# Performance work log

Hardware: AMD Instinct MI355X
Metric: run time of the kernel (lower is better)

Reference implementation:

```python
import jax, jax.numpy as jnp
import numpy as np
import math

H = 16          # num_heads
DN = 128        # qk_nope_head_dim
DR = 64         # qk_rope_head_dim
DV = 128        # v_head_dim
Q_LORA = 1536
KV_LORA = 512
EPS = 1e-6
ROPE_BASE = 10000.0
YARN_FACTOR = 16.0
ORIG_MAX = 8192


def rmsnorm(x, w):
    return x * jax.lax.rsqrt(jnp.mean(x * x, axis=-1, keepdims=True) + EPS) * w


def rotate_half(x):
    h = x.shape[-1] // 2
    return jnp.concatenate([-x[..., h:], x[..., :h]], axis=-1)


def yarn_cos_sin(L, dtype):
    # YaRN-scaled inverse frequencies (RotaryEmbedding defaults)
    pos2 = jnp.arange(0, DR, 2, dtype=jnp.float32)
    inv_freq = 1.0 / (ROPE_BASE ** (pos2 / DR))
    wavelen = 2.0 * jnp.pi / inv_freq
    # low_freq_factor=1.0, high_freq_factor=4.0
    ramp = jnp.clip((ORIG_MAX / wavelen - 1.0) / (4.0 - 1.0), 0.0, 1.0)
    inv_freq = inv_freq * (1.0 - ramp) + (inv_freq / YARN_FACTOR) * ramp
    t = jnp.arange(L, dtype=jnp.float32)
    freqs = jnp.outer(t, inv_freq)                      # [L, DR/2]
    emb = jnp.concatenate([freqs, freqs], axis=-1)      # [L, DR]
    attn_factor = 0.1 * math.log(YARN_FACTOR) + 1.0     # yarn attention scaling
    cos = (jnp.cos(emb) * attn_factor)[None, :, None, :].astype(dtype)
    sin = (jnp.sin(emb) * attn_factor)[None, :, None, :].astype(dtype)
    return cos, sin


def setup_inputs() -> dict:
    key = jax.random.key(0)
    ks = jax.random.split(key, 8)
    s = 0.02
    hid = 2048
    return {
        "x": jax.random.normal(ks[0], (2, 2048, hid), jnp.float32),
        "w_qa": jax.random.normal(ks[1], (hid, Q_LORA), jnp.float32) * s,
        "q_norm_w": jnp.ones((Q_LORA,), jnp.float32),
        "w_qb": jax.random.normal(ks[2], (Q_LORA, H * (DN + DR)), jnp.float32) * s,
        "w_kva": jax.random.normal(ks[3], (hid, KV_LORA + DR), jnp.float32) * s,
        "kv_norm_w": jnp.ones((KV_LORA,), jnp.float32),
        "w_kvb": jax.random.normal(ks[4], (KV_LORA, H * (DN + DV)), jnp.float32) * s,
        "w_o": jax.random.normal(ks[5], (H * DV, hid), jnp.float32) * s,
    }


def reference(x, w_qa, q_norm_w, w_qb, w_kva, kv_norm_w, w_kvb, w_o):
    B, L, _ = x.shape
    # --- low-rank Q path ---
    q = rmsnorm(x @ w_qa, q_norm_w) @ w_qb               # [B, L, H*(DN+DR)]
    q = q.reshape(B, L, H, DN + DR)
    q_nope, q_rope = q[..., :DN], q[..., DN:]
    # --- low-rank KV path ---
    kv = x @ w_kva                                       # [B, L, KV_LORA+DR]
    kv_c, k_rope = kv[..., :KV_LORA], kv[..., KV_LORA:]
    kv = rmsnorm(kv_c, kv_norm_w) @ w_kvb                # [B, L, H*(DN+DV)]
    kv = kv.reshape(B, L, H, DN + DV)
    k_nope, v = kv[..., :DN], kv[..., DN:]
    k_rope = jnp.broadcast_to(k_rope[:, :, None, :], (B, L, H, DR))
    # --- decoupled RoPE on rope sub-dims ---
    cos, sin = yarn_cos_sin(L, x.dtype)
    q_rope = q_rope * cos + rotate_half(q_rope) * sin
    k_rope = k_rope * cos + rotate_half(k_rope) * sin
    q = jnp.concatenate([q_nope, q_rope], axis=-1)       # [B, L, H, DN+DR]
    k = jnp.concatenate([k_nope, k_rope], axis=-1)
    # --- causal SDPA, scale = 1/sqrt(qk head dim) ---
    scale = 1.0 / math.sqrt(DN + DR)
    scores = jnp.einsum('blhd,bmhd->bhlm', q, k) * scale
    mask = jnp.tril(jnp.ones((L, L), bool))
    scores = jnp.where(mask[None, None], scores, jnp.array(-1e30, scores.dtype))
    attn = jax.nn.softmax(scores, axis=-1)
    out = jnp.einsum('bhlm,bmhd->blhd', attn, v)         # [B, L, H, DV]
    return out.reshape(B, L, H * DV) @ w_o               # [B, L, hidden]
```

## Files before the change

### kernel.cpp

```cpp
#include <hip/hip_runtime.h>
#include <hip/hip_bf16.h>
#include <math.h>

#define H_    16
#define B_    2
#define L_    2048
#define HID_  2048
#define QL_   1536
#define KVL_  512

typedef unsigned short u16;
typedef __attribute__((ext_vector_type(8))) short bf16x8;
typedef __attribute__((ext_vector_type(4))) float f32x4;

__device__ __forceinline__ float bf2f(u16 u) {
    unsigned int x = ((unsigned int)u) << 16;
    return __uint_as_float(x);
}
__device__ __forceinline__ u16 f2bf(float f) {
    __hip_bfloat16 b = __float2bfloat16(f);
    return *(u16*)&b;
}
__device__ __forceinline__ void g2l16(const void* g, void* l) {
    __builtin_amdgcn_global_load_lds(
        (const __attribute__((address_space(1))) unsigned int*)g,
        (__attribute__((address_space(3))) unsigned int*)l,
        16, 0, 0);
}
__device__ __forceinline__ int kswz(int l, int d) {
    return (((d >> 3) ^ (l & 7)) << 3) | (d & 7);
}

#define QSCALE (0.07216878364870323f * 1.4426950408889634f)

__device__ inline void yarn_cs(int l, int j, float& c, float& s)
{
    float invf = expf(-(float)(2 * j) * (9.210340371976184f / 64.f));
    float wavelen = 6.283185307179586f / invf;
    float ramp = (8192.f / wavelen - 1.f) * (1.f / 3.f);
    ramp = fminf(fmaxf(ramp, 0.f), 1.f);
    float invf2 = invf * (1.f - ramp) + invf * (1.f / 16.f) * ramp;
    float ang = (float)l * invf2;
    const float af = 1.2772588722239781f;
    c = cosf(ang) * af;
    s = sinf(ang) * af;
}

__global__ __launch_bounds__(256) void yarn_tab(float* __restrict__ tab)
{
    int idx = blockIdx.x * 256 + threadIdx.x;
    int l = idx >> 5, j = idx & 31;
    float c, s; yarn_cs(l, j, c, s);
    tab[l * 64 + j] = c;
    tab[l * 64 + 32 + j] = s;
}

__global__ __launch_bounds__(256) void cvt_bf16(
    const float* __restrict__ in, u16* __restrict__ outp)
{
    int idx = blockIdx.x * 256 + threadIdx.x;
    float4 a = ((const float4*)in)[idx * 2];
    float4 b = ((const float4*)in)[idx * 2 + 1];
    union { uint4 v; u16 s[8]; } u;
    u.s[0] = f2bf(a.x); u.s[1] = f2bf(a.y); u.s[2] = f2bf(a.z); u.s[3] = f2bf(a.w);
    u.s[4] = f2bf(b.x); u.s[5] = f2bf(b.y); u.s[6] = f2bf(b.z); u.s[7] = f2bf(b.w);
    ((uint4*)outp)[idx] = u.v;
}

__global__ __launch_bounds__(256) void wtrans(
    const float* __restrict__ W, u16* __restrict__ Wt, int K, int N,
    const float* __restrict__ wvec)
{
    __shared__ float t[64][65];
    const int n0 = blockIdx.x * 64, k0 = blockIdx.y * 64;
    const int tid = threadIdx.x;
    {
        int lr = tid >> 2, nc = (tid & 3) * 16;
        float wk = wvec ? wvec[k0 + lr] : 1.f;
        const float* src = W + (size_t)(k0 + lr) * N + n0 + nc;
#pragma unroll
        for (int j = 0; j < 16; j += 4) {
            float4 v = *(const float4*)(src + j);
            t[lr][nc + j] = v.x * wk; t[lr][nc + j + 1] = v.y * wk;
            t[lr][nc + j + 2] = v.z * wk; t[lr][nc + j + 3] = v.w * wk;
        }
    }
    __syncthreads();
    {
        int nr = tid >> 2, kc = (tid & 3) * 16;
        union { uint4 v[2]; u16 s[16]; } u;
#pragma unroll
        for (int j = 0; j < 16; ++j) u.s[j] = f2bf(t[kc + j][nr]);
        uint4* dst = (uint4*)(Wt + (size_t)(n0 + nr) * K + k0 + kc);
        dst[0] = u.v[0]; dst[1] = u.v[1];
    }
}

__global__ __launch_bounds__(256) void rowss(
    const u16* __restrict__ in, int stride, int ncols, float* __restrict__ sc)
{
    const int row = blockIdx.x, tid = threadIdx.x;
    const u16* ir = in + (size_t)row * stride;
    const int nch = ncols >> 3;
    float ss = 0.f;
    for (int c = tid; c < nch; c += 256) {
        union { uint4 v; u16 s[8]; } u;
        u.v = *(const uint4*)(ir + c * 8);
#pragma unroll
        for (int j = 0; j < 8; ++j) { float v = bf2f(u.s[j]); ss += v * v; }
    }
#pragma unroll
    for (int o = 32; o > 0; o >>= 1) ss += __shfl_xor(ss, o);
    __shared__ float red[4];
    if ((tid & 63) == 0) red[tid >> 6] = ss;
    __syncthreads();
    if (tid == 0) {
        float tot = red[0] + red[1] + red[2] + red[3];
        sc[row] = rsqrtf(tot / (float)ncols + 1e-6f);
    }
}

template<int NI> struct EpiStoreF32 {
    float* C; int ldc;
    __device__ void operator()(const f32x4* acc, int m0, int n0, int wr, int wc,
                               int g, int n) const {
#pragma unroll
        for (int mi = 0; mi < 4; ++mi)
#pragma unroll
            for (int ni = 0; ni < NI; ++ni)
#pragma unroll
                for (int i = 0; i < 4; ++i)
                    C[(size_t)(m0 + wr + mi * 16 + g * 4 + i) * ldc
                      + n0 + wc + ni * 16 + n] = acc[mi * NI + ni][i];
    }
};
struct EpiQA {
    u16* qaR; u16* kvf;
    __device__ void operator()(const f32x4* acc, int m0, int n0, int wr, int wc,
                               int g, int n) const {
        int c0 = n0 + wc;
#pragma unroll
        for (int mi = 0; mi < 4; ++mi)
#pragma unroll
            for (int i = 0; i < 4; ++i) {
                int rr = m0 + wr + mi * 16 + g * 4 + i;
#pragma unroll
                for (int ni = 0; ni < 4; ++ni) {
                    int c = c0 + ni * 16 + n;
                    float v = acc[mi * 4 + ni][i];
                    if (c < 1536)      qaR[(size_t)rr * 1536 + c] = f2bf(v);
                    else if (c < 2112) kvf[(size_t)rr * 576 + (c - 1536)] = f2bf(v);
                }
            }
    }
};
struct EpiQ {
    u16* Qb; const float* tab; const float* sc;
    __device__ void operator()(const f32x4* acc, int m0, int n0, int wr, int wc,
                               int g, int n) const {
        int c0 = n0 + wc;
        int h = c0 / 192, r0 = c0 % 192;
#pragma unroll
        for (int mi = 0; mi < 4; ++mi)
#pragma unroll
            for (int i = 0; i < 4; ++i) {
                int rr = m0 + wr + mi * 16 + g * 4 + i;
                int b = rr >> 11, l = rr & 2047;
                float scl = sc[rr] * QSCALE;
                size_t base = ((size_t)(b * 16 + h) * 2048 + l) * 192;
                if (r0 < 128) {
#pragma unroll
                    for (int ni = 0; ni < 4; ++ni)
                        Qb[base + r0 + ni * 16 + n] = f2bf(acc[mi * 4 + ni][i] * scl);
                } else {
#pragma unroll
                    for (int ni = 0; ni < 2; ++ni) {
                        int j = ni * 16 + n;
                        float cs = tab[l * 64 + j], sn = tab[l * 64 + 32 + j];
                        float lo = acc[mi * 4 + ni][i] * scl;
                        float hi = acc[mi * 4 + ni + 2][i] * scl;
                        Qb[base + 128 + j] = f2bf(lo * cs - hi * sn);
                        Qb[base + 160 + j] = f2bf(hi * cs + lo * sn);
                    }
                }
            }
    }
};
struct EpiKV {
    u16* Kb; u16* Vc; const float* sc;
    __device__ void operator()(const f32x4* acc, int m0, int n0, int wr, int wc,
                               int g, int n) const {
        int c0 = n0 + wc;
        int h = c0 >> 8, r0 = c0 & 255;
#pragma unroll
        for (int mi = 0; mi < 4; ++mi)
#pragma unroll
            for (int i = 0; i < 4; ++i) {
                int rr = m0 + wr + mi * 16 + g * 4 + i;
                int b = rr >> 11, l = rr & 2047;
                float scl = sc[rr];
                if (r0 < 128) {
                    size_t base = ((size_t)(b * 16 + h) * 2048 + l) * 192;
#pragma unroll
                    for (int ni = 0; ni < 4; ++ni) {
                        int d = r0 + ni * 16 + n;
                        Kb[base + kswz(l, d)] = f2bf(acc[mi * 4 + ni][i] * scl);
                    }
                } else {
#pragma unroll
                    for (int ni = 0; ni < 4; ++ni)
                        Vc[(size_t)rr * 2048 + h * 128 + (r0 - 128) + ni * 16 + n]
                            = f2bf(acc[mi * 4 + ni][i] * scl);
                }
            }
    }
};

template<int BN, class Epi>
__global__ __launch_bounds__(256) void gemm_bf16(
    const u16* __restrict__ A, int lda,
    const u16* __restrict__ Bt, int ldb,
    int K, Epi epi)
{
    constexpr int NI = BN / 32;
    __shared__ u16 As[128 * 32];
    __shared__ u16 Bs[BN * 32];
    const int tid = threadIdx.x;
    const int w = tid >> 6, lane = tid & 63;
    const int g = lane >> 4, n = lane & 15;
    const int wr = (w >> 1) * 64, wc = (w & 1) * (BN / 2);
    const int nwg = gridDim.x * gridDim.y;
    const int lin = blockIdx.y * gridDim.x + blockIdx.x;
    const int swz = (lin & 7) * (nwg >> 3) + (lin >> 3);
    const int m0 = (swz / gridDim.x) * 128, n0 = (swz % gridDim.x) * BN;
    const int arow = lane >> 2, acol = (lane & 3) * 8;

    f32x4 acc[4][NI];
#pragma unroll
    for (int mi = 0; mi < 4; ++mi)
#pragma unroll
        for (int ni = 0; ni < NI; ++ni) acc[mi][ni] = (f32x4){0.f, 0.f, 0.f, 0.f};

    for (int k0 = 0; k0 < K; k0 += 32) {
        __syncthreads();
#pragma unroll
        for (int i = 0; i < 2; ++i) {
            int seg = w * 2 + i;
            int row = seg * 16 + arow;
            g2l16(A + (size_t)(m0 + row) * lda + k0 + acol, &As[seg * 512]);
        }
        if constexpr (BN == 128) {
#pragma unroll
            for (int i = 0; i < 2; ++i) {
                int seg = w * 2 + i;
                int row = seg * 16 + arow;
                g2l16(Bt + (size_t)(n0 + row) * ldb + k0 + acol, &Bs[seg * 512]);
            }
        } else {
            int row = w * 16 + arow;
            g2l16(Bt + (size_t)(n0 + row) * ldb + k0 + acol, &Bs[w * 512]);
        }
        __syncthreads();

        bf16x8 af[4], bf[NI];
#pragma unroll
        for (int mi = 0; mi < 4; ++mi)
            af[mi] = *(const bf16x8*)&As[(wr + mi * 16 + n) * 32 + g * 8];
#pragma unroll
        for (int ni = 0; ni < NI; ++ni)
            bf[ni] = *(const bf16x8*)&Bs[(wc + ni * 16 + n) * 32 + g * 8];
#pragma unroll
        for (int mi = 0; mi < 4; ++mi)
#pragma unroll
            for (int ni = 0; ni < NI; ++ni)
                acc[mi][ni] = __builtin_amdgcn_mfma_f32_16x16x32_bf16(
                    af[mi], bf[ni], acc[mi][ni], 0, 0, 0);
    }
    epi(&acc[0][0], m0, n0, wr, wc, g, n);
}

__global__ __launch_bounds__(256) void krope(
    const u16* __restrict__ kvf_b, u16* __restrict__ Kb,
    const float* __restrict__ tab)
{
    int idx = blockIdx.x * 256 + threadIdx.x;
    int j = idx & 31;
    int l = (idx >> 5) & 2047;
    int bh = idx >> 16;
    int b = bh >> 4;
    size_t row = (size_t)(b * 2048 + l);
    float x0 = bf2f(kvf_b[row * 576 + 512 + j]);
    float x1 = bf2f(kvf_b[row * 576 + 544 + j]);
    float cs = tab[l * 64 + j], sn = tab[l * 64 + 32 + j];
    size_t base = ((size_t)bh * 2048 + l) * 192;
    Kb[base + kswz(l, 128 + j)] = f2bf(x0 * cs - x1 * sn);
    Kb[base + kswz(l, 160 + j)] = f2bf(x1 * cs + x0 * sn);
}

__global__ __launch_bounds__(256) void vtrans_b(
    const u16* __restrict__ Vc, u16* __restrict__ Vt)
{
    __shared__ u16 t[64][72];
    const int tid = threadIdx.x;
    const int bh = blockIdx.z, b = bh >> 4, h = bh & 15;
    const int l0 = blockIdx.x * 64, dv0 = blockIdx.y * 64;
    {
        int lr = tid >> 2, dc = (tid & 3) * 16;
        const u16* src = Vc + (size_t)(b * 2048 + l0 + lr) * 2048 + h * 128 + dv0 + dc;
        uint4 v0 = *(const uint4*)src;
        uint4 v1 = *(const uint4*)(src + 8);
        *(uint4*)&t[lr][dc] = v0;
        *(uint4*)&t[lr][dc + 8] = v1;
    }
    __syncthreads();
    {
        int dvr = tid >> 2, lc = (tid & 3) * 16;
        union { uint4 v[2]; u16 s[16]; } u;
#pragma unroll
        for (int j = 0; j < 16; ++j) u.s[j] = t[lc + j][dvr];
        uint4* dst = (uint4*)(Vt + ((size_t)bh * 128 + dv0 + dvr) * 2048 + l0 + lc);
        dst[0] = u.v[0]; dst[1] = u.v[1];
    }
}

__global__ __launch_bounds__(256) void attn_mfma(
    const u16* __restrict__ Qb,
    const u16* __restrict__ Kb,
    const u16* __restrict__ Vt,
    u16* __restrict__ outp)
{
    __shared__ u16 Kl[64 * 192];
    __shared__ u16 Vl[128 * 64];

    const int tid = threadIdx.x;
    const int w = tid >> 6, lane = tid & 63;
    const int g = lane >> 4, n = lane & 15;
    const int n7 = n & 7;
    const int lin = blockIdx.x;
    const int xcd = lin & 7, j = lin >> 3;
    const int qt = 31 - (j >> 2);
    const int bh = xcd * 4 + (j & 3);
    const int b = bh >> 4;
    const int qb0 = qt << 6;

    u16* PtW = Kl + w * 1280;

    const u16* KsrcBase = Kb + (size_t)bh * L_ * 192;
    const u16* VsrcBase = Vt + (size_t)bh * 128 * 2048;

    bf16x8 qf[6];
    {
        const int qrow = qb0 + w * 16 + n;
        const u16* qp = Qb + ((size_t)bh * L_ + qrow) * 192 + g * 8;
#pragma unroll
        for (int kk = 0; kk < 6; ++kk)
            qf[kk] = *(const bf16x8*)(qp + kk * 32);
    }

    f32x4 acc[8];
#pragma unroll
    for (int dt = 0; dt < 8; ++dt) acc[dt] = (f32x4){0.f, 0.f, 0.f, 0.f};
    float li[4] = {0.f, 0.f, 0.f, 0.f};

    const int ntiles = qt + 1;
    for (int kt = 0; kt < ntiles; ++kt) {
        const int kb = kt << 6;
        __syncthreads();
        {
            const u16* Ksrc = KsrcBase + (size_t)kb * 192;
#pragma unroll
            for (int i = 0; i < 6; ++i) {
                int c = i * 4 + w;
                g2l16(Ksrc + c * 512 + lane * 8, &Kl[c * 512]);
            }
        }
        {
#pragma unroll
            for (int i = 0; i < 4; ++i) {
                int c = i * 4 + w;
                int dv = c * 8 + (lane >> 3);
                int blk = (lane & 7) ^ (lane >> 3);
                g2l16(VsrcBase + (size_t)dv * 2048 + kb + blk * 8, &Vl[c * 512]);
            }
        }
        __syncthreads();

        f32x4 s[4];
#pragma unroll
        for (int c = 0; c < 4; ++c) s[c] = (f32x4){0.f, 0.f, 0.f, 0.f};
        __builtin_amdgcn_s_setprio(1);
#pragma unroll
        for (int c = 0; c < 4; ++c)
#pragma unroll
            for (int kk = 0; kk < 6; ++kk) {
                bf16x8 kf = *(const bf16x8*)
                    &Kl[(c * 16 + n) * 192 + ((kk * 4 + g) ^ n7) * 8];
                s[c] = __builtin_amdgcn_mfma_f32_16x16x32_bf16(qf[kk], kf, s[c], 0, 0, 0);
            }
        __builtin_amdgcn_s_setprio(0);

        const bool diag = (kt == qt);
#pragma unroll
        for (int i = 0; i < 4; ++i) {
            float v[4];
            if (diag) {
                int qr = qb0 + w * 16 + g * 4 + i;
#pragma unroll
                for (int c = 0; c < 4; ++c)
                    v[c] = (kb + c * 16 + n <= qr) ? s[c][i] : -1e30f;
            } else {
#pragma unroll
                for (int c = 0; c < 4; ++c) v[c] = s[c][i];
            }
            float p0 = __builtin_amdgcn_exp2f(v[0]);
            float p1 = __builtin_amdgcn_exp2f(v[1]);
            float p2 = __builtin_amdgcn_exp2f(v[2]);
            float p3 = __builtin_amdgcn_exp2f(v[3]);
            li[i] += (p0 + p1) + (p2 + p3);
            s[0][i] = p0; s[1][i] = p1; s[2][i] = p2; s[3][i] = p3;
        }

        __syncthreads();

#pragma unroll
        for (int c = 0; c < 4; ++c) {
            union { double d; u16 hh[4]; } u;
#pragma unroll
            for (int i = 0; i < 4; ++i) u.hh[i] = f2bf(s[c][i]);
            *(double*)&PtW[(c * 16 + n) * 20 + g * 4] = u.d;
        }
        asm volatile("s_waitcnt lgkmcnt(0)" ::: "memory");
        __builtin_amdgcn_sched_barrier(0);

        union { bf16x8 v; short e[8]; } pf[2];
#pragma unroll
        for (int ks = 0; ks < 2; ++ks)
#pragma unroll
            for (int jj = 0; jj < 8; ++jj)
                pf[ks].e[jj] = *(const short*)&PtW[(ks * 32 + g * 8 + jj) * 20 + n];

        __builtin_amdgcn_s_setprio(1);
#pragma unroll
        for (int dt = 0; dt < 8; ++dt) {
#pragma unroll
            for (int ks = 0; ks < 2; ++ks) {
                bf16x8 vf = *(const bf16x8*)
                    &Vl[(dt * 16 + n) * 64 + (((ks * 4 + g) ^ n7) << 3)];
                acc[dt] = __builtin_amdgcn_mfma_f32_16x16x32_bf16(pf[ks].v, vf, acc[dt], 0, 0, 0);
            }
        }
        __builtin_amdgcn_s_setprio(0);
    }

    float inv[4];
#pragma unroll
    for (int i = 0; i < 4; ++i) {
        float t = li[i];
        t += __shfl_xor(t, 1);
        t += __shfl_xor(t, 2);
        t += __shfl_xor(t, 4);
        t += __shfl_xor(t, 8);
        inv[i] = __frcp_rn(t);
    }
#pragma unroll
    for (int dt = 0; dt < 8; ++dt) {
#pragma unroll
        for (int i = 0; i < 4; ++i) {
            int qr = qb0 + w * 16 + g * 4 + i;
            outp[(size_t)(b * L_ + qr) * 2048 + (bh & 15) * 128 + dt * 16 + n]
                = f2bf(acc[dt][i] * inv[i]);
        }
    }
}

extern "C" void kernel_launch(void* const* d_in, const int* in_sizes, int n_in,
                              void* d_out, int out_size, void* d_ws, size_t ws_size,
                              hipStream_t stream)
{
    const float* x     = (const float*)d_in[0];
    const float* w_qa  = (const float*)d_in[1];
    const float* qnw   = (const float*)d_in[2];
    const float* w_qb  = (const float*)d_in[3];
    const float* w_kva = (const float*)d_in[4];
    const float* kvnw  = (const float*)d_in[5];
    const float* w_kvb = (const float*)d_in[6];
    const float* w_o   = (const float*)d_in[7];
    float* out = (float*)d_out;
    u16* W = (u16*)d_ws;

    const size_t o_wt_qa  = 0;
    const size_t o_wt_qb  = (size_t)2176 * 2048;
    const size_t o_wt_kvb = o_wt_qb  + (size_t)3072 * 1536;
    const size_t o_wt_o   = o_wt_kvb + (size_t)4096 * 512;
    const size_t o_tab    = o_wt_o   + (size_t)2048 * 2048;
    const size_t o_sc     = o_tab    + 262144;
    const size_t o_Qb     = o_sc     + 16384;
    const size_t o_Kb     = o_Qb     + 12582912;
    const size_t o_Vt     = o_Kb     + 12582912;
    const size_t o_Vc     = o_Vt     + 8388608;
    const size_t o_xb     = o_Vc     + 8388608;

    u16* Wt_qa  = W + o_wt_qa;
    u16* Wt_kva = W + o_wt_qa + (size_t)1536 * 2048;
    u16* Wt_qb  = W + o_wt_qb;
    u16* Wt_kvb = W + o_wt_kvb;
    u16* Wt_o   = W + o_wt_o;
    float* tab  = (float*)(W + o_tab);
    float* sc_q  = (float*)(W + o_sc);
    float* sc_kv = sc_q + 4096;
    u16* Qb     = W + o_Qb;
    u16* qaR_b  = W + o_Kb;
    u16* Kb     = W + o_Kb;
    u16* kvf_b  = W + o_Vt;
    u16* Vt     = W + o_Vt;
    u16* Vc     = W + o_Vc;
    u16* atto_b = W + o_Vc;
    u16* x_b    = W + o_xb;

    dim3 blk(256);

    yarn_tab<<<(2048 * 32) / 256, blk, 0, stream>>>(tab);
    cvt_bf16<<<4096, blk, 0, stream>>>(x, x_b);
    wtrans<<<dim3(1536 / 64, 2048 / 64), blk, 0, stream>>>(w_qa,  Wt_qa,  2048, 1536, nullptr);
    wtrans<<<dim3( 576 / 64, 2048 / 64), blk, 0, stream>>>(w_kva, Wt_kva, 2048, 576,  nullptr);
    wtrans<<<dim3(3072 / 64, 1536 / 64), blk, 0, stream>>>(w_qb,  Wt_qb,  1536, 3072, qnw);
    wtrans<<<dim3(4096 / 64,  512 / 64), blk, 0, stream>>>(w_kvb, Wt_kvb, 512, 4096,  kvnw);
    wtrans<<<dim3(2048 / 64, 2048 / 64), blk, 0, stream>>>(w_o,   Wt_o,   2048, 2048, nullptr);

    gemm_bf16<128, EpiQA><<<dim3(17, 32), blk, 0, stream>>>(
        x_b, 2048, Wt_qa, 2048, 2048, EpiQA{qaR_b, kvf_b});
    rowss<<<4096, blk, 0, stream>>>(qaR_b, 1536, 1536, sc_q);
    rowss<<<4096, blk, 0, stream>>>(kvf_b, 576, 512, sc_kv);
    gemm_bf16<128, EpiQ><<<dim3(24, 32), blk, 0, stream>>>(
        qaR_b, 1536, Wt_qb, 1536, 1536, EpiQ{Qb, tab, sc_q});
    gemm_bf16<128, EpiKV><<<dim3(32, 32), blk, 0, stream>>>(
        kvf_b, 576, Wt_kvb, 512, 512, EpiKV{Kb, Vc, sc_kv});
    krope<<<(32 * 2048 * 32) / 256, blk, 0, stream>>>(kvf_b, Kb, tab);
    vtrans_b<<<dim3(32, 2, 32), blk, 0, stream>>>(Vc, Vt);

    attn_mfma<<<dim3(1024), blk, 0, stream>>>(Qb, Kb, Vt, atto_b);
    gemm_bf16<128, EpiStoreF32<4>><<<dim3(16, 32), blk, 0, stream>>>(
        atto_b, 2048, Wt_o, 2048, 2048, EpiStoreF32<4>{out, 2048});
}
```

Before: 334.4 us.

## Merge independent kernels into combined launches to cut launch count

Folds the five weight-transpose launches into one, the two row-norm launches into one, the Q-up and KV-up GEMMs into one grid dispatched by block id, and krope plus V-transpose into one kernel. This removes launch gaps and tail bubbles between small independent kernels and lets their blocks share the GPU. The GEMM template is fixed to BN=128 with a 1-D grid and explicit column-tile count; branching by block id adds some divergence-free dispatch overhead.

Measured after the change: 306.2 us. 1.09x faster.

```diff
diff --git a/kernel.cpp b/kernel.cpp
--- a/kernel.cpp
+++ b/kernel.cpp
@@ -67,12 +67,24 @@
     ((uint4*)outp)[idx] = u.v;
 }
 
-__global__ __launch_bounds__(256) void wtrans(
-    const float* __restrict__ W, u16* __restrict__ Wt, int K, int N,
-    const float* __restrict__ wvec)
+__global__ __launch_bounds__(256) void wtrans_all(
+    const float* __restrict__ w_qa, const float* __restrict__ w_kva,
+    const float* __restrict__ w_qb, const float* __restrict__ w_kvb,
+    const float* __restrict__ w_o,
+    u16* __restrict__ Wt_qa, u16* __restrict__ Wt_kva, u16* __restrict__ Wt_qb,
+    u16* __restrict__ Wt_kvb, u16* __restrict__ Wt_o,
+    const float* __restrict__ qnw, const float* __restrict__ kvnw)
 {
     __shared__ float t[64][65];
-    const int n0 = blockIdx.x * 64, k0 = blockIdx.y * 64;
+    int bid = blockIdx.x;
+    const float* W; u16* Wt; int K, N; const float* wvec = nullptr; int loc;
+    if (bid < 768)       { W = w_qa;  Wt = Wt_qa;  K = 2048; N = 1536; loc = bid; }
+    else if (bid < 1056) { W = w_kva; Wt = Wt_kva; K = 2048; N = 576;  loc = bid - 768; }
+    else if (bid < 2208) { W = w_qb;  Wt = Wt_qb;  K = 1536; N = 3072; wvec = qnw;  loc = bid - 1056; }
+    else if (bid < 2720) { W = w_kvb; Wt = Wt_kvb; K = 512;  N = 4096; wvec = kvnw; loc = bid - 2208; }
+    else                 { W = w_o;   Wt = Wt_o;   K = 2048; N = 2048; loc = bid - 2720; }
+    const int nx = N >> 6;
+    const int n0 = (loc % nx) * 64, k0 = (loc / nx) * 64;
     const int tid = threadIdx.x;
     {
         int lr = tid >> 2, nc = (tid & 3) * 16;
@@ -96,11 +108,16 @@
     }
 }
 
-__global__ __launch_bounds__(256) void rowss(
-    const u16* __restrict__ in, int stride, int ncols, float* __restrict__ sc)
-{
-    const int row = blockIdx.x, tid = threadIdx.x;
-    const u16* ir = in + (size_t)row * stride;
+__global__ __launch_bounds__(256) void rowss2(
+    const u16* __restrict__ qaR, const u16* __restrict__ kvf,
+    float* __restrict__ sc_q, float* __restrict__ sc_kv)
+{
+    __shared__ float red[4];
+    int row = blockIdx.x;
+    const u16* ir; int ncols; float* outp;
+    if (row < 4096) { ir = qaR + (size_t)row * 1536; ncols = 1536; outp = sc_q + row; }
+    else { row -= 4096; ir = kvf + (size_t)row * 576; ncols = 512; outp = sc_kv + row; }
+    const int tid = threadIdx.x;
     const int nch = ncols >> 3;
     float ss = 0.f;
     for (int c = tid; c < nch; c += 256) {
@@ -111,12 +128,11 @@
     }
 #pragma unroll
     for (int o = 32; o > 0; o >>= 1) ss += __shfl_xor(ss, o);
-    __shared__ float red[4];
     if ((tid & 63) == 0) red[tid >> 6] = ss;
     __syncthreads();
     if (tid == 0) {
         float tot = red[0] + red[1] + red[2] + red[3];
-        sc[row] = rsqrtf(tot / (float)ncols + 1e-6f);
+        *outp = rsqrtf(tot / (float)ncols + 1e-6f);
     }
 }
 
@@ -216,30 +232,26 @@
     }
 };
 
-template<int BN, class Epi>
-__global__ __launch_bounds__(256) void gemm_bf16(
+template<class Epi>
+__device__ __forceinline__ void gemm_body(
+    u16* As, u16* Bs,
     const u16* __restrict__ A, int lda,
     const u16* __restrict__ Bt, int ldb,
-    int K, Epi epi)
-{
-    constexpr int NI = BN / 32;
-    __shared__ u16 As[128 * 32];
-    __shared__ u16 Bs[BN * 32];
+    int K, Epi epi, int lin, int nwg, int nx)
+{
     const int tid = threadIdx.x;
     const int w = tid >> 6, lane = tid & 63;
     const int g = lane >> 4, n = lane & 15;
-    const int wr = (w >> 1) * 64, wc = (w & 1) * (BN / 2);
-    const int nwg = gridDim.x * gridDim.y;
-    const int lin = blockIdx.y * gridDim.x + blockIdx.x;
+    const int wr = (w >> 1) * 64, wc = (w & 1) * 64;
     const int swz = (lin & 7) * (nwg >> 3) + (lin >> 3);
-    const int m0 = (swz / gridDim.x) * 128, n0 = (swz % gridDim.x) * BN;
+    const int m0 = (swz / nx) * 128, n0 = (swz % nx) * 128;
     const int arow = lane >> 2, acol = (lane & 3) * 8;
 
-    f32x4 acc[4][NI];
+    f32x4 acc[4][4];
 #pragma unroll
     for (int mi = 0; mi < 4; ++mi)
 #pragma unroll
-        for (int ni = 0; ni < NI; ++ni) acc[mi][ni] = (f32x4){0.f, 0.f, 0.f, 0.f};
+        for (int ni = 0; ni < 4; ++ni) acc[mi][ni] = (f32x4){0.f, 0.f, 0.f, 0.f};
 
     for (int k0 = 0; k0 < K; k0 += 32) {
         __syncthreads();
@@ -249,61 +261,82 @@
             int row = seg * 16 + arow;
             g2l16(A + (size_t)(m0 + row) * lda + k0 + acol, &As[seg * 512]);
         }
-        if constexpr (BN == 128) {
-#pragma unroll
-            for (int i = 0; i < 2; ++i) {
-                int seg = w * 2 + i;
-                int row = seg * 16 + arow;
-                g2l16(Bt + (size_t)(n0 + row) * ldb + k0 + acol, &Bs[seg * 512]);
-            }
-        } else {
-            int row = w * 16 + arow;
-            g2l16(Bt + (size_t)(n0 + row) * ldb + k0 + acol, &Bs[w * 512]);
+#pragma unroll
+        for (int i = 0; i < 2; ++i) {
+            int seg = w * 2 + i;
+            int row = seg * 16 + arow;
+            g2l16(Bt + (size_t)(n0 + row) * ldb + k0 + acol, &Bs[seg * 512]);
         }
         __syncthreads();
 
-        bf16x8 af[4], bf[NI];
+        bf16x8 af[4], bf[4];
 #pragma unroll
         for (int mi = 0; mi < 4; ++mi)
             af[mi] = *(const bf16x8*)&As[(wr + mi * 16 + n) * 32 + g * 8];
 #pragma unroll
-        for (int ni = 0; ni < NI; ++ni)
+        for (int ni = 0; ni < 4; ++ni)
             bf[ni] = *(const bf16x8*)&Bs[(wc + ni * 16 + n) * 32 + g * 8];
 #pragma unroll
         for (int mi = 0; mi < 4; ++mi)
 #pragma unroll
-            for (int ni = 0; ni < NI; ++ni)
+            for (int ni = 0; ni < 4; ++ni)
                 acc[mi][ni] = __builtin_amdgcn_mfma_f32_16x16x32_bf16(
                     af[mi], bf[ni], acc[mi][ni], 0, 0, 0);
     }
     epi(&acc[0][0], m0, n0, wr, wc, g, n);
 }
 
-__global__ __launch_bounds__(256) void krope(
+template<class Epi>
+__global__ __launch_bounds__(256) void gemm_bf16(
+    const u16* __restrict__ A, int lda,
+    const u16* __restrict__ Bt, int ldb,
+    int K, Epi epi, int nx)
+{
+    __shared__ u16 As[128 * 32];
+    __shared__ u16 Bs[128 * 32];
+    gemm_body<Epi>(As, Bs, A, lda, Bt, ldb, K, epi, blockIdx.x, gridDim.x, nx);
+}
+
+__global__ __launch_bounds__(256) void gemm_qkv(
+    const u16* __restrict__ qaR, const u16* __restrict__ Wt_qb, EpiQ eq,
+    const u16* __restrict__ kvf, const u16* __restrict__ Wt_kvb, EpiKV ekv)
+{
+    __shared__ u16 As[128 * 32];
+    __shared__ u16 Bs[128 * 32];
+    int bid = blockIdx.x;
+    if (bid < 768)
+        gemm_body<EpiQ>(As, Bs, qaR, 1536, Wt_qb, 1536, 1536, eq, bid, 768, 24);
+    else
+        gemm_body<EpiKV>(As, Bs, kvf, 576, Wt_kvb, 512, 512, ekv, bid - 768, 1024, 32);
+}
+
+__global__ __launch_bounds__(256) void krope_vtrans(
     const u16* __restrict__ kvf_b, u16* __restrict__ Kb,
-    const float* __restrict__ tab)
-{
-    int idx = blockIdx.x * 256 + threadIdx.x;
-    int j = idx & 31;
-    int l = (idx >> 5) & 2047;
-    int bh = idx >> 16;
-    int b = bh >> 4;
-    size_t row = (size_t)(b * 2048 + l);
-    float x0 = bf2f(kvf_b[row * 576 + 512 + j]);
-    float x1 = bf2f(kvf_b[row * 576 + 544 + j]);
-    float cs = tab[l * 64 + j], sn = tab[l * 64 + 32 + j];
-    size_t base = ((size_t)bh * 2048 + l) * 192;
-    Kb[base + kswz(l, 128 + j)] = f2bf(x0 * cs - x1 * sn);
-    Kb[base + kswz(l, 160 + j)] = f2bf(x1 * cs + x0 * sn);
-}
-
-__global__ __launch_bounds__(256) void vtrans_b(
+    const float* __restrict__ tab,
     const u16* __restrict__ Vc, u16* __restrict__ Vt)
 {
     __shared__ u16 t[64][72];
+    int bid = blockIdx.x;
+    if (bid < 8192) {
+        int idx = bid * 256 + threadIdx.x;
+        int j = idx & 31;
+        int l = (idx >> 5) & 2047;
+        int bh = idx >> 16;
+        int b = bh >> 4;
+        size_t row = (size_t)(b * 2048 + l);
+        float x0 = bf2f(kvf_b[row * 576 + 512 + j]);
+        float x1 = bf2f(kvf_b[row * 576 + 544 + j]);
+        float cs = tab[l * 64 + j], sn = tab[l * 64 + 32 + j];
+        size_t base = ((size_t)bh * 2048 + l) * 192;
+        Kb[base + kswz(l, 128 + j)] = f2bf(x0 * cs - x1 * sn);
+        Kb[base + kswz(l, 160 + j)] = f2bf(x1 * cs + x0 * sn);
+        return;
+    }
+    int vb = bid - 8192;
+    const int bh = vb & 31, b = bh >> 4, h = bh & 15;
+    const int dv0 = ((vb >> 5) & 1) * 64;
+    const int l0 = (vb >> 6) * 64;
     const int tid = threadIdx.x;
-    const int bh = blockIdx.z, b = bh >> 4, h = bh & 15;
-    const int l0 = blockIdx.x * 64, dv0 = blockIdx.y * 64;
     {
         int lr = tid >> 2, dc = (tid & 3) * 16;
         const u16* src = Vc + (size_t)(b * 2048 + l0 + lr) * 2048 + h * 128 + dv0 + dc;
@@ -521,24 +554,19 @@
 
     yarn_tab<<<(2048 * 32) / 256, blk, 0, stream>>>(tab);
     cvt_bf16<<<4096, blk, 0, stream>>>(x, x_b);
-    wtrans<<<dim3(1536 / 64, 2048 / 64), blk, 0, stream>>>(w_qa,  Wt_qa,  2048, 1536, nullptr);
-    wtrans<<<dim3( 576 / 64, 2048 / 64), blk, 0, stream>>>(w_kva, Wt_kva, 2048, 576,  nullptr);
-    wtrans<<<dim3(3072 / 64, 1536 / 64), blk, 0, stream>>>(w_qb,  Wt_qb,  1536, 3072, qnw);
-    wtrans<<<dim3(4096 / 64,  512 / 64), blk, 0, stream>>>(w_kvb, Wt_kvb, 512, 4096,  kvnw);
-    wtrans<<<dim3(2048 / 64, 2048 / 64), blk, 0, stream>>>(w_o,   Wt_o,   2048, 2048, nullptr);
-
-    gemm_bf16<128, EpiQA><<<dim3(17, 32), blk, 0, stream>>>(
-        x_b, 2048, Wt_qa, 2048, 2048, EpiQA{qaR_b, kvf_b});
-    rowss<<<4096, blk, 0, stream>>>(qaR_b, 1536, 1536, sc_q);
-    rowss<<<4096, blk, 0, stream>>>(kvf_b, 576, 512, sc_kv);
-    gemm_bf16<128, EpiQ><<<dim3(24, 32), blk, 0, stream>>>(
-        qaR_b, 1536, Wt_qb, 1536, 1536, EpiQ{Qb, tab, sc_q});
-    gemm_bf16<128, EpiKV><<<dim3(32, 32), blk, 0, stream>>>(
-        kvf_b, 576, Wt_kvb, 512, 512, EpiKV{Kb, Vc, sc_kv});
-    krope<<<(32 * 2048 * 32) / 256, blk, 0, stream>>>(kvf_b, Kb, tab);
-    vtrans_b<<<dim3(32, 2, 32), blk, 0, stream>>>(Vc, Vt);
+    wtrans_all<<<3744, blk, 0, stream>>>(
+        w_qa, w_kva, w_qb, w_kvb, w_o,
+        Wt_qa, Wt_kva, Wt_qb, Wt_kvb, Wt_o, qnw, kvnw);
+
+    gemm_bf16<EpiQA><<<544, blk, 0, stream>>>(
+        x_b, 2048, Wt_qa, 2048, 2048, EpiQA{qaR_b, kvf_b}, 17);
+    rowss2<<<8192, blk, 0, stream>>>(qaR_b, kvf_b, sc_q, sc_kv);
+    gemm_qkv<<<1792, blk, 0, stream>>>(
+        qaR_b, Wt_qb, EpiQ{Qb, tab, sc_q},
+        kvf_b, Wt_kvb, EpiKV{Kb, Vc, sc_kv});
+    krope_vtrans<<<10240, blk, 0, stream>>>(kvf_b, Kb, tab, Vc, Vt);
 
     attn_mfma<<<dim3(1024), blk, 0, stream>>>(Qb, Kb, Vt, atto_b);
-    gemm_bf16<128, EpiStoreF32<4>><<<dim3(16, 32), blk, 0, stream>>>(
-        atto_b, 2048, Wt_o, 2048, 2048, EpiStoreF32<4>{out, 2048});
-}
+    gemm_bf16<EpiStoreF32<4>><<<512, blk, 0, stream>>>(
+        atto_b, 2048, Wt_o, 2048, 2048, EpiStoreF32<4>{out, 2048}, 16);
+}
```
